# Kernel optimization log

Hardware: AMD Instinct MI355X
Metric: run time of the kernel (lower is better)

The kernel has to match this reference:

```python
import jax, jax.numpy as jnp
import numpy as np

DIM = 1024
N_SLOTS = 8
RANK = 256
T = 1024
B = 8
SPECTRAL_RADIUS = 0.99


def setup_inputs() -> dict:
    key = jax.random.key(0)
    ks = jax.random.split(key, 6)
    x = jax.random.normal(ks[0], (T, B, DIM), dtype=jnp.float32)
    z = jax.random.normal(ks[1], (T, B, DIM), dtype=jnp.float32)
    h0 = jnp.zeros((B, N_SLOTS, DIM), dtype=jnp.float32)
    # parameters (xavier-ish / scaled as in _init_weights)
    W_x = jax.random.normal(ks[2], (DIM, DIM), dtype=jnp.float32) * (1.0 / np.sqrt(DIM))
    U = jax.random.normal(ks[3], (N_SLOTS, DIM, RANK), dtype=jnp.float32) * (SPECTRAL_RADIUS * 0.3 / np.sqrt(DIM))
    V = jax.random.normal(ks[4], (N_SLOTS, RANK, DIM), dtype=jnp.float32) * (0.5 / np.sqrt(DIM))
    b = jnp.zeros((DIM,), dtype=jnp.float32)
    C = jnp.ones((N_SLOTS,), dtype=jnp.float32) / N_SLOTS
    return {"x": x, "z": z, "h0": h0, "W_x": W_x, "U": U, "V": V, "b": b, "C": C}


def reference(x, z, h0, W_x, U, V, b, C):
    # x, z: [T, B, D]; h0: [B, S, D]
    def step(h_prev, xz):
        x_t, z_t = xz                               # [B, D] each
        Wx = x_t @ W_x.T                            # [B, D]
        Vh = jnp.einsum('bsd,srd->bsr', h_prev, V)  # [B, S, R]
        Uh = jnp.einsum('bsr,sdr->bsd', Vh, U)      # [B, S, D]
        h_new = jnp.tanh(Wx[:, None, :] + Uh + b)   # [B, S, D]
        h_comb = jnp.einsum('bsd,s->bd', h_new, C)  # [B, D]
        out = h_comb * jax.nn.silu(z_t)             # [B, D]
        return h_new, (h_new, out)

    _, (hs, output) = jax.lax.scan(step, h0, (x, z))
    # hs: [T, B, S, D]; prepend h0 -> [T+1, B, S, D] -> permute to [T+1, S, B, D]
    h = jnp.concatenate([h0[None], hs], axis=0)
    h = jnp.transpose(h, (0, 2, 1, 3))
    return output, h
```

## Files before the change

kernel.cpp:

```cpp
#include <hip/hip_runtime.h>
#include <cstdint>
#include <cstddef>

#define DIM 1024
#define NS 8
#define RANK 256
#define TSTEPS 1024
#define BB 8
#define NG 8
#define DCH 128

typedef __attribute__((ext_vector_type(8))) short s8v;
typedef __attribute__((ext_vector_type(4))) short s4v;
typedef __attribute__((ext_vector_type(4))) float f4v;
typedef __attribute__((ext_vector_type(2))) float f2v;

__device__ __forceinline__ unsigned short f2bf(float f) {
  unsigned u = __float_as_uint(f);
  u += 0x7fffu + ((u >> 16) & 1u);
  return (unsigned short)(u >> 16);
}
__device__ __forceinline__ float bf2f(unsigned short h) {
  return __uint_as_float(((unsigned)h) << 16);
}

__global__ void init_kernel(const float* __restrict__ h0, float* __restrict__ hOut0,
                            unsigned int* __restrict__ tags) {
  int i = blockIdx.x * blockDim.x + threadIdx.x;
  const int NH = NS * BB * DIM;
  if (i < NH) {
    int s = i >> 13, b = (i >> 10) & 7, d = i & 1023;
    hOut0[i] = h0[((size_t)b * NS + s) * DIM + d];
  }
  if (i < 128) tags[i] = 0u;
}

__global__ __launch_bounds__(256) void gemm_wx(const float* __restrict__ X,
                                               const float* __restrict__ W,
                                               float* __restrict__ Co) {
  __shared__ unsigned short As[128][40];
  __shared__ unsigned short Bh[128][40];
  __shared__ unsigned short Bl[128][40];
  const int bn = blockIdx.x & 7;
  const int bm = blockIdx.x >> 3;
  const int tid = threadIdx.x;
  const int wave = tid >> 6, lane = tid & 63, l15 = lane & 15, quad = lane >> 4;
  const int wm = wave & 1, wn = wave >> 1;
  f4v acc[4][4];
  for (int i = 0; i < 4; ++i)
    for (int j = 0; j < 4; ++j) acc[i][j] = (f4v){0.f, 0.f, 0.f, 0.f};
  const int row = tid >> 1, kh = (tid & 1) * 16;
  const float* srcA = X + ((size_t)(bm * 128 + row)) * DIM + kh;
  const float* srcB = W + ((size_t)(bn * 128 + row)) * DIM + kh;
  for (int k0 = 0; k0 < DIM; k0 += 32) {
    __syncthreads();
    unsigned short ta[16], th[16], tl[16];
    for (int q = 0; q < 16; q += 4) {
      f4v a4 = *(const f4v*)(srcA + k0 + q);
      for (int r2 = 0; r2 < 4; ++r2) ta[q + r2] = f2bf(a4[r2]);
      f4v b4 = *(const f4v*)(srcB + k0 + q);
      for (int r2 = 0; r2 < 4; ++r2) {
        unsigned short hi = f2bf(b4[r2]);
        th[q + r2] = hi;
        tl[q + r2] = f2bf(b4[r2] - bf2f(hi));
      }
    }
    *(s8v*)&As[row][kh] = *(s8v*)&ta[0];
    *(s8v*)&As[row][kh + 8] = *(s8v*)&ta[8];
    *(s8v*)&Bh[row][kh] = *(s8v*)&th[0];
    *(s8v*)&Bh[row][kh + 8] = *(s8v*)&th[8];
    *(s8v*)&Bl[row][kh] = *(s8v*)&tl[0];
    *(s8v*)&Bl[row][kh + 8] = *(s8v*)&tl[8];
    __syncthreads();
    s8v af[4], bhf[4], blf[4];
    for (int i = 0; i < 4; ++i) af[i] = *(const s8v*)&As[wm * 64 + i * 16 + l15][quad * 8];
    for (int j = 0; j < 4; ++j) bhf[j] = *(const s8v*)&Bh[wn * 64 + j * 16 + l15][quad * 8];
    for (int j = 0; j < 4; ++j) blf[j] = *(const s8v*)&Bl[wn * 64 + j * 16 + l15][quad * 8];
    for (int i = 0; i < 4; ++i)
      for (int j = 0; j < 4; ++j) {
        acc[i][j] = __builtin_amdgcn_mfma_f32_16x16x32_bf16(af[i], bhf[j], acc[i][j], 0, 0, 0);
        acc[i][j] = __builtin_amdgcn_mfma_f32_16x16x32_bf16(af[i], blf[j], acc[i][j], 0, 0, 0);
      }
  }
  for (int i = 0; i < 4; ++i)
    for (int j = 0; j < 4; ++j) {
      int ci = bm * 128 + wm * 64 + i * 16 + quad * 4;
      int cd = bn * 128 + wn * 64 + j * 16 + l15;
      for (int r2 = 0; r2 < 4; ++r2)
        Co[((size_t)(ci + r2)) * DIM + cd] = acc[i][j][r2];
    }
}

__global__ __launch_bounds__(256) void seq_kernel(const float* __restrict__ Wx,
                                                  float* __restrict__ hOut,
                                                  const float* __restrict__ bias,
                                                  const float* __restrict__ U,
                                                  const float* __restrict__ V,
                                                  const float* __restrict__ h0,
                                                  float* __restrict__ vx,
                                                  unsigned int* __restrict__ tags) {
  const int s = blockIdx.x & 7;
  const int g = blockIdx.x >> 3;
  const int tid = threadIdx.x;
  const int wave = tid >> 6, lane = tid & 63, l15 = lane & 15, quad = lane >> 4;
  const int d0 = g * DCH;

  __shared__ unsigned short hbuf[16][DCH + 8];
  __shared__ unsigned short vbuf[16][RANK + 8];

  s8v Vfrag[4][4];
  #pragma unroll
  for (int mt = 0; mt < 4; ++mt)
    #pragma unroll
    for (int kk = 0; kk < 4; ++kk) {
      const float* p = V + ((size_t)s * RANK + wave * 64 + mt * 16 + l15) * DIM
                         + d0 + kk * 32 + quad * 8;
      s8v f;
      #pragma unroll
      for (int j = 0; j < 8; ++j) f[j] = (short)f2bf(p[j]);
      Vfrag[mt][kk] = f;
    }
  s8v Ufrag[2][8];
  #pragma unroll
  for (int mt = 0; mt < 2; ++mt)
    #pragma unroll
    for (int kk = 0; kk < 8; ++kk) {
      const float* p = U + ((size_t)s * DIM + d0 + wave * 32 + mt * 16 + l15) * RANK
                         + kk * 32 + quad * 8;
      s8v f;
      #pragma unroll
      for (int j = 0; j < 8; ++j) f[j] = (short)f2bf(p[j]);
      Ufrag[mt][kk] = f;
    }
  float bias4[2][4];
  #pragma unroll
  for (int mt = 0; mt < 2; ++mt)
    #pragma unroll
    for (int r2 = 0; r2 < 4; ++r2)
      bias4[mt][r2] = bias[d0 + wave * 32 + mt * 16 + quad * 4 + r2];

  for (int c = tid; c < BB * DCH; c += 256) {
    int b = c >> 7, dl = c & 127;
    hbuf[b][dl] = f2bf(h0[((size_t)b * NS + s) * DIM + d0 + dl]);
  }
  __syncthreads();

  const int b_ep = l15;
  const int bpoll = tid >> 5;
  const int rbase = (tid & 31) * 8;

  for (int t = 0; t < TSTEPS; ++t) {
    const int buf = t & 1;
    const unsigned want = (unsigned)(t + 1);

    f4v wx4[2];
    if (b_ep < 8) {
      #pragma unroll
      for (int mt = 0; mt < 2; ++mt)
        wx4[mt] = *(const f4v*)&Wx[((size_t)t * BB + b_ep) * DIM + d0 + wave * 32 + mt * 16 + quad * 4];
    }

    f4v acc1[4];
    #pragma unroll
    for (int mt = 0; mt < 4; ++mt) acc1[mt] = (f4v){0.f, 0.f, 0.f, 0.f};
    #pragma unroll
    for (int kk = 0; kk < 4; ++kk) {
      s8v hfrag = *(const s8v*)&hbuf[l15][kk * 32 + quad * 8];
      #pragma unroll
      for (int mt = 0; mt < 4; ++mt)
        acc1[mt] = __builtin_amdgcn_mfma_f32_16x16x32_bf16(Vfrag[mt][kk], hfrag, acc1[mt], 0, 0, 0);
    }

    if (b_ep < 8) {
      unsigned long long* vw = (unsigned long long*)vx
          + ((size_t)(s * 2 + buf) * NG + g) * 1024 + (size_t)b_ep * 128;
      #pragma unroll
      for (int mt = 0; mt < 4; ++mt) {
        int half = wave * 32 + mt * 8 + quad * 2;
        union { f2v f; unsigned long long u; } c0, c1;
        c0.f = (f2v){acc1[mt][0], acc1[mt][1]};
        c1.f = (f2v){acc1[mt][2], acc1[mt][3]};
        __hip_atomic_store(vw + half, c0.u, __ATOMIC_RELAXED, __HIP_MEMORY_SCOPE_AGENT);
        __hip_atomic_store(vw + half + 1, c1.u, __ATOMIC_RELAXED, __HIP_MEMORY_SCOPE_AGENT);
      }
    }
    asm volatile("s_waitcnt vmcnt(0)" ::: "memory");
    __syncthreads();
    if (tid == 0)
      __hip_atomic_store(tags + (s * 2 + buf) * NG + g, want,
                         __ATOMIC_RELAXED, __HIP_MEMORY_SCOPE_AGENT);

    {
      const unsigned int* tg = tags + (s * 2 + buf) * NG;
      for (;;) {
        unsigned bad = 0;
        #pragma unroll
        for (int g2 = 0; g2 < NG; ++g2)
          bad |= __hip_atomic_load(tg + g2, __ATOMIC_RELAXED, __HIP_MEMORY_SCOPE_AGENT) ^ want;
        if (!bad) break;
      }
    }
    asm volatile("" ::: "memory");

    {
      const unsigned long long* vr = (const unsigned long long*)vx
          + ((size_t)(s * 2 + buf) * NG) * 1024 + (size_t)bpoll * 128 + (tid & 31) * 4;
      float sum[8] = {0.f, 0.f, 0.f, 0.f, 0.f, 0.f, 0.f, 0.f};
      #pragma unroll
      for (int g2 = 0; g2 < NG; ++g2) {
        #pragma unroll
        for (int q = 0; q < 4; ++q) {
          unsigned long long u = __hip_atomic_load(vr + (size_t)g2 * 1024 + q,
                                                   __ATOMIC_RELAXED, __HIP_MEMORY_SCOPE_AGENT);
          union { unsigned long long u; f2v f; } c; c.u = u;
          sum[q * 2] += c.f[0];
          sum[q * 2 + 1] += c.f[1];
        }
      }
      s8v v8;
      #pragma unroll
      for (int j = 0; j < 8; ++j) v8[j] = (short)f2bf(sum[j]);
      *(s8v*)&vbuf[bpoll][rbase] = v8;
    }
    __syncthreads();

    f4v acc2[2];
    acc2[0] = (f4v){0.f, 0.f, 0.f, 0.f};
    acc2[1] = (f4v){0.f, 0.f, 0.f, 0.f};
    #pragma unroll
    for (int kk = 0; kk < 8; ++kk) {
      s8v vfrag = *(const s8v*)&vbuf[l15][kk * 32 + quad * 8];
      acc2[0] = __builtin_amdgcn_mfma_f32_16x16x32_bf16(Ufrag[0][kk], vfrag, acc2[0], 0, 0, 0);
      acc2[1] = __builtin_amdgcn_mfma_f32_16x16x32_bf16(Ufrag[1][kk], vfrag, acc2[1], 0, 0, 0);
    }
    if (b_ep < 8) {
      #pragma unroll
      for (int mt = 0; mt < 2; ++mt) {
        int dl = wave * 32 + mt * 16 + quad * 4;
        f4v h4;
        s4v hb;
        #pragma unroll
        for (int r2 = 0; r2 < 4; ++r2) {
          float u = acc2[mt][r2] + wx4[mt][r2] + bias4[mt][r2];
          u = fminf(fmaxf(u, -15.f), 15.f);
          float e = __expf(2.f * u);
          float hv = (e - 1.f) / (e + 1.f);
          h4[r2] = hv;
          hb[r2] = (short)f2bf(hv);
        }
        *(f4v*)&hOut[(((size_t)(t + 1) * NS + s) * BB + b_ep) * DIM + d0 + dl] = h4;
        *(s4v*)&hbuf[b_ep][dl] = hb;
      }
    }
    __syncthreads();
  }
}

__global__ void out_kernel(const float* __restrict__ z, const float* __restrict__ h,
                           const float* __restrict__ Cs, float* __restrict__ out) {
  size_t i = (size_t)blockIdx.x * blockDim.x + threadIdx.x;
  const size_t n4 = (size_t)TSTEPS * BB * DIM / 4;
  float c[8];
  for (int s2 = 0; s2 < 8; ++s2) c[s2] = Cs[s2];
  for (; i < n4; i += (size_t)gridDim.x * blockDim.x) {
    size_t base = i * 4;
    size_t t = base / (BB * DIM);
    size_t rem = base % (BB * DIM);
    f4v accv = (f4v){0.f, 0.f, 0.f, 0.f};
    for (int s2 = 0; s2 < 8; ++s2) {
      f4v hv = *(const f4v*)&h[((t + 1) * NS + s2) * (size_t)(BB * DIM) + rem];
      accv += hv * c[s2];
    }
    f4v zv = *(const f4v*)&z[base];
    f4v o;
    for (int r2 = 0; r2 < 4; ++r2) {
      float zz = zv[r2];
      float sil = zz / (1.f + __expf(-zz));
      o[r2] = accv[r2] * sil;
    }
    *(f4v*)&out[base] = o;
  }
}

extern "C" void kernel_launch(void* const* d_in, const int* in_sizes, int n_in,
                              void* d_out, int out_size, void* d_ws, size_t ws_size,
                              hipStream_t stream) {
  const float* x  = (const float*)d_in[0];
  const float* z  = (const float*)d_in[1];
  const float* h0 = (const float*)d_in[2];
  const float* Wm = (const float*)d_in[3];
  const float* U  = (const float*)d_in[4];
  const float* V  = (const float*)d_in[5];
  const float* bs = (const float*)d_in[6];
  const float* Cs = (const float*)d_in[7];

  float* out  = (float*)d_out;
  float* hOut = out + (size_t)TSTEPS * BB * DIM;

  float* vx = (float*)d_ws;
  unsigned int* tags = (unsigned int*)(vx + (size_t)NS * 2 * NG * BB * RANK);

  float* Wx = out;

  init_kernel<<<256, 256, 0, stream>>>(h0, hOut, tags);
  gemm_wx<<<512, 256, 0, stream>>>(x, Wm, Wx);
  seq_kernel<<<64, 256, 0, stream>>>(Wx, hOut, bs, U, V, h0, vx, tags);
  out_kernel<<<2048, 256, 0, stream>>>(z, hOut, Cs, out);
}
```

Measured before the change: 4.873 ms.

## Replace tag-based barrier with per-value step tags packed into partial-sum words

Each partial Vh value is now stored as a 64-bit word that holds the float together with the current step tag. Consumers poll those words directly until every group's tag matches. This removes the separate tag flags, the vmcnt wait, the block barrier before publishing and the extra round trip of flag polling. In exchange it doubles the bytes written and polled per partial and keeps 64 values in registers, and the launch bound is now set for one block per SM.

After: 9.884 ms. 2.03x slower.

```diff
diff --git a/kernel.cpp b/kernel.cpp
--- a/kernel.cpp
+++ b/kernel.cpp
@@ -13,7 +13,6 @@
 typedef __attribute__((ext_vector_type(8))) short s8v;
 typedef __attribute__((ext_vector_type(4))) short s4v;
 typedef __attribute__((ext_vector_type(4))) float f4v;
-typedef __attribute__((ext_vector_type(2))) float f2v;
 
 __device__ __forceinline__ unsigned short f2bf(float f) {
   unsigned u = __float_as_uint(f);
@@ -25,14 +24,15 @@
 }
 
 __global__ void init_kernel(const float* __restrict__ h0, float* __restrict__ hOut0,
-                            unsigned int* __restrict__ tags) {
+                            unsigned long long* __restrict__ vx) {
   int i = blockIdx.x * blockDim.x + threadIdx.x;
   const int NH = NS * BB * DIM;
   if (i < NH) {
     int s = i >> 13, b = (i >> 10) & 7, d = i & 1023;
     hOut0[i] = h0[((size_t)b * NS + s) * DIM + d];
   }
-  if (i < 128) tags[i] = 0u;
+  #pragma unroll
+  for (int k = 0; k < 4; ++k) vx[(size_t)i * 4 + k] = 0ull;
 }
 
 __global__ __launch_bounds__(256) void gemm_wx(const float* __restrict__ X,
@@ -91,14 +91,13 @@
     }
 }
 
-__global__ __launch_bounds__(256) void seq_kernel(const float* __restrict__ Wx,
-                                                  float* __restrict__ hOut,
-                                                  const float* __restrict__ bias,
-                                                  const float* __restrict__ U,
-                                                  const float* __restrict__ V,
-                                                  const float* __restrict__ h0,
-                                                  float* __restrict__ vx,
-                                                  unsigned int* __restrict__ tags) {
+__global__ __launch_bounds__(256, 1) void seq_kernel(const float* __restrict__ Wx,
+                                                     float* __restrict__ hOut,
+                                                     const float* __restrict__ bias,
+                                                     const float* __restrict__ U,
+                                                     const float* __restrict__ V,
+                                                     const float* __restrict__ h0,
+                                                     unsigned long long* __restrict__ vx) {
   const int s = blockIdx.x & 7;
   const int g = blockIdx.x >> 3;
   const int tid = threadIdx.x;
@@ -172,51 +171,53 @@
     }
 
     if (b_ep < 8) {
-      unsigned long long* vw = (unsigned long long*)vx
-          + ((size_t)(s * 2 + buf) * NG + g) * 1024 + (size_t)b_ep * 128;
+      unsigned long long* vw = vx + ((size_t)(s * 2 + buf) * NG + g) * (BB * RANK)
+                                  + (size_t)b_ep * RANK;
       #pragma unroll
       for (int mt = 0; mt < 4; ++mt) {
-        int half = wave * 32 + mt * 8 + quad * 2;
-        union { f2v f; unsigned long long u; } c0, c1;
-        c0.f = (f2v){acc1[mt][0], acc1[mt][1]};
-        c1.f = (f2v){acc1[mt][2], acc1[mt][3]};
-        __hip_atomic_store(vw + half, c0.u, __ATOMIC_RELAXED, __HIP_MEMORY_SCOPE_AGENT);
-        __hip_atomic_store(vw + half + 1, c1.u, __ATOMIC_RELAXED, __HIP_MEMORY_SCOPE_AGENT);
-      }
-    }
-    asm volatile("s_waitcnt vmcnt(0)" ::: "memory");
-    __syncthreads();
-    if (tid == 0)
-      __hip_atomic_store(tags + (s * 2 + buf) * NG + g, want,
-                         __ATOMIC_RELAXED, __HIP_MEMORY_SCOPE_AGENT);
-
-    {
-      const unsigned int* tg = tags + (s * 2 + buf) * NG;
-      for (;;) {
-        unsigned bad = 0;
-        #pragma unroll
-        for (int g2 = 0; g2 < NG; ++g2)
-          bad |= __hip_atomic_load(tg + g2, __ATOMIC_RELAXED, __HIP_MEMORY_SCOPE_AGENT) ^ want;
-        if (!bad) break;
-      }
-    }
-    asm volatile("" ::: "memory");
-
-    {
-      const unsigned long long* vr = (const unsigned long long*)vx
-          + ((size_t)(s * 2 + buf) * NG) * 1024 + (size_t)bpoll * 128 + (tid & 31) * 4;
-      float sum[8] = {0.f, 0.f, 0.f, 0.f, 0.f, 0.f, 0.f, 0.f};
-      #pragma unroll
-      for (int g2 = 0; g2 < NG; ++g2) {
-        #pragma unroll
-        for (int q = 0; q < 4; ++q) {
-          unsigned long long u = __hip_atomic_load(vr + (size_t)g2 * 1024 + q,
-                                                   __ATOMIC_RELAXED, __HIP_MEMORY_SCOPE_AGENT);
-          union { unsigned long long u; f2v f; } c; c.u = u;
-          sum[q * 2] += c.f[0];
-          sum[q * 2 + 1] += c.f[1];
+        int r = wave * 64 + mt * 16 + quad * 4;
+        #pragma unroll
+        for (int r2 = 0; r2 < 4; ++r2) {
+          unsigned long long pk = ((unsigned long long)want << 32)
+                                | (unsigned long long)__float_as_uint(acc1[mt][r2]);
+          __hip_atomic_store(vw + r + r2, pk, __ATOMIC_RELAXED, __HIP_MEMORY_SCOPE_AGENT);
         }
       }
+    }
+    asm volatile("" ::: "memory");
+
+    {
+      const unsigned long long* vr = vx + (size_t)(s * 2 + buf) * NG * (BB * RANK)
+                                        + (size_t)bpoll * RANK + rbase;
+      unsigned long long vals[64];
+      unsigned pend = (1u << NG) - 1u;
+      do {
+        #pragma unroll
+        for (int g2 = 0; g2 < NG; ++g2)
+          if (pend & (1u << g2)) {
+            #pragma unroll
+            for (int q = 0; q < 8; ++q)
+              vals[g2 * 8 + q] = __hip_atomic_load(vr + (size_t)g2 * (BB * RANK) + q,
+                                                   __ATOMIC_RELAXED, __HIP_MEMORY_SCOPE_AGENT);
+          }
+        #pragma unroll
+        for (int g2 = 0; g2 < NG; ++g2)
+          if (pend & (1u << g2)) {
+            unsigned long long bad = 0ull;
+            #pragma unroll
+            for (int q = 0; q < 8; ++q)
+              bad |= (vals[g2 * 8 + q] >> 32) ^ (unsigned long long)want;
+            if (!bad) pend &= ~(1u << g2);
+          }
+      } while (pend);
+      float sum[8];
+      #pragma unroll
+      for (int q = 0; q < 8; ++q) sum[q] = 0.f;
+      #pragma unroll
+      for (int g2 = 0; g2 < NG; ++g2)
+        #pragma unroll
+        for (int q = 0; q < 8; ++q)
+          sum[q] += __uint_as_float((unsigned)vals[g2 * 8 + q]);
       s8v v8;
       #pragma unroll
       for (int j = 0; j < 8; ++j) v8[j] = (short)f2bf(sum[j]);
@@ -297,13 +298,12 @@
   float* out  = (float*)d_out;
   float* hOut = out + (size_t)TSTEPS * BB * DIM;
 
-  float* vx = (float*)d_ws;
-  unsigned int* tags = (unsigned int*)(vx + (size_t)NS * 2 * NG * BB * RANK);
+  unsigned long long* vx = (unsigned long long*)d_ws;
 
   float* Wx = out;
 
-  init_kernel<<<256, 256, 0, stream>>>(h0, hOut, tags);
+  init_kernel<<<256, 256, 0, stream>>>(h0, hOut, vx);
   gemm_wx<<<512, 256, 0, stream>>>(x, Wm, Wx);
-  seq_kernel<<<64, 256, 0, stream>>>(Wx, hOut, bs, U, V, h0, vx, tags);
+  seq_kernel<<<64, 256, 0, stream>>>(Wx, hOut, bs, U, V, h0, vx);
   out_kernel<<<2048, 256, 0, stream>>>(z, hOut, Cs, out);
 }
```
